# Optimization experiments

Measured on AMD Instinct MI355X. Metric: run time of the kernel, lower is better.

## Reference

```python
import jax, jax.numpy as jnp
import numpy as np

B, S, D = 2, 2048, 4096
NH, NKV = 32, 8
HD = D // NH          # 128
NREP = NH // NKV      # 4
THETA = 10000.0


def _rope_tables(seq_len, head_dim):
    inv = 1.0 / (THETA ** (jnp.arange(0, head_dim, 2, dtype=jnp.float32) / head_dim))  # [HD/2]
    t = jnp.arange(seq_len, dtype=jnp.float32)
    ang = jnp.outer(t, inv)                      # [S, HD/2]
    return jnp.cos(ang), jnp.sin(ang)


def _apply_rope(x, cos, sin):
    # x: [b, s, h, d]; interleaved pairs (even=real, odd=imag), matching view_as_complex
    xr = x.reshape(*x.shape[:-1], HD // 2, 2)
    x0, x1 = xr[..., 0], xr[..., 1]
    c = cos[None, :, None, :]
    s = sin[None, :, None, :]
    o0 = x0 * c - x1 * s
    o1 = x0 * s + x1 * c
    return jnp.stack([o0, o1], axis=-1).reshape(x.shape)


def setup_inputs() -> dict:
    key = jax.random.key(0)
    ks = jax.random.split(key, 5)
    sc = 0.02
    return {
        "x": jax.random.normal(ks[0], (B, S, D), jnp.float32),
        "wq": jax.random.normal(ks[1], (D, NH * HD), jnp.float32) * sc,
        "wk": jax.random.normal(ks[2], (D, NKV * HD), jnp.float32) * sc,
        "wv": jax.random.normal(ks[3], (D, NKV * HD), jnp.float32) * sc,
        "wo": jax.random.normal(ks[4], (NH * HD, D), jnp.float32) * sc,
        "start_pos": 0,
        "inference": 0,
    }


def reference(x, wq, wk, wv, wo, start_pos, inference):
    bsz, seq_len, _ = x.shape
    # QKV projections (training path: inference=False)
    xq = (x @ wq).reshape(bsz, seq_len, NH, HD)
    xk = (x @ wk).reshape(bsz, seq_len, NKV, HD)
    xv = (x @ wv).reshape(bsz, seq_len, NKV, HD)

    cos, sin = _rope_tables(seq_len, HD)
    xq = _apply_rope(xq, cos, sin)
    xk = _apply_rope(xk, cos, sin)

    # GQA without materializing repeated KV: group q heads per kv head
    q = xq.reshape(bsz, seq_len, NKV, NREP, HD)           # [b, s, g, r, d]
    scores = jnp.einsum('bqgrd,bkgd->bgrqk', q, xk) / np.sqrt(HD)
    causal = jnp.triu(jnp.full((seq_len, seq_len), -jnp.inf, jnp.float32), k=1)
    scores = scores + causal
    probs = jax.nn.softmax(scores.astype(jnp.float32), axis=-1).astype(x.dtype)
    out = jnp.einsum('bgrqk,bkgd->bqgrd', probs, xv)      # [b, s, g, r, d]
    out = out.reshape(bsz, seq_len, NH * HD)
    return out @ wo
```

## Files before the change

kernel.cpp:

```cpp
#include <hip/hip_runtime.h>
#include <hip/hip_bf16.h>

#define B_ 2
#define S_ 2048
#define D_ 4096
#define NH_ 32
#define NKV_ 8
#define HD_ 128
#define NREP_ 4

typedef unsigned short u16;
typedef __attribute__((ext_vector_type(8))) short short8;
typedef __attribute__((ext_vector_type(4))) float f32x4;

__device__ inline float bf2f(u16 u) {
    union { unsigned u; float f; } v; v.u = ((unsigned)u) << 16; return v.f;
}
__device__ inline u16 f2bf(float f) {
    union { float f; unsigned u; } v; v.f = f;
    unsigned r = v.u + 0x7fffu + ((v.u >> 16) & 1u);
    return (u16)(r >> 16);
}
__device__ inline unsigned cvt_pk(float lo, float hi) {
    unsigned r;
    asm("v_cvt_pk_bf16_f32 %0, %1, %2" : "=v"(r) : "v"(lo), "v"(hi));
    return r;
}
__device__ inline float exp2_fast(float x) {
    float r;
    asm("v_exp_f32 %0, %1" : "=v"(r) : "v"(x));
    return r;
}

__device__ inline void gl_lds16(const u16* g, u16* l) {
    __builtin_amdgcn_global_load_lds(
        (const __attribute__((address_space(1))) unsigned int*)g,
        (__attribute__((address_space(3))) unsigned int*)l, 16, 0, 0);
}

__global__ __launch_bounds__(256) void conv_k(const float* __restrict__ in,
                                              u16* __restrict__ out) {
    size_t i = ((size_t)blockIdx.x * 256 + threadIdx.x) * 4;
    float4 v = *(const float4*)&in[i];
    uint2 t;
    t.x = cvt_pk(v.x, v.y);
    t.y = cvt_pk(v.z, v.w);
    *(uint2*)&out[i] = t;
}

__global__ __launch_bounds__(256) void tconv_k(const float* __restrict__ in,
                                               u16* __restrict__ out,
                                               int R, int C) {
    __shared__ u16 tile[64][65];
    int bx = blockIdx.x * 64, by = blockIdx.y * 64;
    int tx = threadIdx.x, ty = threadIdx.y;
    for (int i = ty; i < 64; i += 4)
        tile[i][tx] = f2bf(in[(size_t)(by + i) * C + bx + tx]);
    __syncthreads();
    for (int i = ty; i < 64; i += 4)
        out[(size_t)(bx + i) * R + by + tx] = tile[tx][i];
}

__global__ __launch_bounds__(256) void tconv2_k(const float* __restrict__ in0,
                                                const float* __restrict__ in1,
                                                u16* __restrict__ out0,
                                                u16* __restrict__ out1,
                                                int R, int C) {
    __shared__ u16 tile[64][65];
    const float* in = blockIdx.z ? in1 : in0;
    u16* out = blockIdx.z ? out1 : out0;
    int bx = blockIdx.x * 64, by = blockIdx.y * 64;
    int tx = threadIdx.x, ty = threadIdx.y;
    for (int i = ty; i < 64; i += 4)
        tile[i][tx] = f2bf(in[(size_t)(by + i) * C + bx + tx]);
    __syncthreads();
    for (int i = ty; i < 64; i += 4)
        out[(size_t)(bx + i) * R + by + tx] = tile[tx][i];
}

__global__ __launch_bounds__(256) void transpose_k(const u16* __restrict__ in,
                                                   u16* __restrict__ out,
                                                   int R, int C) {
    __shared__ u16 tile[64][65];
    const u16* ib = in + (size_t)blockIdx.z * R * C;
    u16* ob = out + (size_t)blockIdx.z * R * C;
    int bx = blockIdx.x * 64, by = blockIdx.y * 64;
    int tx = threadIdx.x, ty = threadIdx.y;
    for (int i = ty; i < 64; i += 4)
        tile[i][tx] = ib[(size_t)(by + i) * C + bx + tx];
    __syncthreads();
    for (int i = ty; i < 64; i += 4)
        ob[(size_t)(bx + i) * R + by + tx] = tile[tx][i];
}

__global__ __launch_bounds__(256) void gemm_kv(const u16* __restrict__ A,
                                               const u16* __restrict__ Bt,
                                               u16* __restrict__ Kout,
                                               u16* __restrict__ Vout,
                                               int M, int K) {
    __shared__ __align__(16) u16 As[128 * 32];
    __shared__ __align__(16) u16 Bs[128 * 32];
    int tid = threadIdx.x;
    int w = tid >> 6, lane = tid & 63;
    int ln = lane & 15, qd = lane >> 4;
    int wr = w >> 1, wc = w & 1;
    int m0 = blockIdx.y * 128, n0 = blockIdx.x * 128;

    int srow = lane >> 2;
    int skk  = (lane & 3) * 8;
    const u16* Ag = A  + (size_t)(m0 + w * 32 + srow) * K + skk;
    const u16* Bg = Bt + (size_t)(n0 + w * 32 + srow) * K + skk;

    f32x4 acc[4][4];
#pragma unroll
    for (int i = 0; i < 4; ++i)
#pragma unroll
        for (int j = 0; j < 4; ++j)
            acc[i][j] = f32x4{0.f, 0.f, 0.f, 0.f};

    for (int k0 = 0; k0 < K; k0 += 32) {
#pragma unroll
        for (int t = 0; t < 2; ++t) {
            gl_lds16(Ag + (size_t)(t * 16) * K + k0, &As[(w * 32 + t * 16) * 32]);
            gl_lds16(Bg + (size_t)(t * 16) * K + k0, &Bs[(w * 32 + t * 16) * 32]);
        }
        __syncthreads();
        short8 af[4], bfr[4];
#pragma unroll
        for (int i = 0; i < 4; ++i)
            af[i] = *(const short8*)&As[(wr * 64 + i * 16 + ln) * 32 + qd * 8];
#pragma unroll
        for (int j = 0; j < 4; ++j)
            bfr[j] = *(const short8*)&Bs[(wc * 64 + j * 16 + ln) * 32 + qd * 8];
#pragma unroll
        for (int i = 0; i < 4; ++i)
#pragma unroll
            for (int j = 0; j < 4; ++j)
                acc[i][j] = __builtin_amdgcn_mfma_f32_16x16x32_bf16(af[i], bfr[j], acc[i][j], 0, 0, 0);
        __syncthreads();
    }
    u16* dst = (n0 < 1024) ? Kout : Vout;
    int nb = (n0 < 1024) ? n0 : (n0 - 1024);
#pragma unroll
    for (int i = 0; i < 4; ++i)
#pragma unroll
        for (int j = 0; j < 4; ++j)
#pragma unroll
            for (int r = 0; r < 4; ++r) {
                int row = m0 + wr * 64 + i * 16 + qd * 4 + r;
                int col = nb + wc * 64 + j * 16 + ln;
                dst[(size_t)row * 1024 + col] = f2bf(acc[i][j][r]);
            }
}

__device__ inline short8 lds_frag(const u16* base, int row, int colb) {
    int lin = ((row & 127) << 7) + colb;
    int off = ((row >> 7) << 14) + (lin ^ (((lin >> 9) & 1) << 5));
    return *(const short8*)((const char*)base + off);
}

__device__ inline void stage_half(const u16* g, int row0, int ldK, int k0,
                                  u16* ldsHalf, int w, int lane) {
#pragma unroll
    for (int j = 0; j < 2; ++j) {
        int Lb = (w << 11) + (j << 10) + (lane << 4);
        int src = Lb ^ (((Lb >> 9) & 1) << 5);
        const u16* gp = g + (size_t)(row0 + (src >> 7)) * ldK + k0 + ((src & 127) >> 1);
        gl_lds16(gp, ldsHalf + (((w << 11) + (j << 10)) >> 1));
    }
}

#define PH_MFMA(MB)                                                           \
    asm volatile("s_waitcnt lgkmcnt(0)" ::: "memory");                        \
    __builtin_amdgcn_sched_barrier(0);                                        \
    __builtin_amdgcn_s_setprio(1);                                            \
    _Pragma("unroll") for (int mi = 0; mi < 2; ++mi)                          \
      _Pragma("unroll") for (int ni = 0; ni < 4; ++ni)                        \
        _Pragma("unroll") for (int kk = 0; kk < 2; ++kk)                      \
          acc[(MB) + mi][ni] = __builtin_amdgcn_mfma_f32_16x16x32_bf16(       \
              af[mi][kk], bfr[ni][kk], acc[(MB) + mi][ni], 0, 0, 0);          \
    __builtin_amdgcn_s_setprio(0);                                            \
    __builtin_amdgcn_s_barrier();

#define TILE_BODY(T, CURA, CURB, OTHA)                                        \
  {                                                                           \
    const int t_ = (T);                                                       \
    const bool p1_ = (t_ + 1 < nt), p2_ = (t_ + 2 < nt);                      \
    short8 bfr[4][2], af[2][2];                                               \
    _Pragma("unroll") for (int ni = 0; ni < 4; ++ni)                          \
      _Pragma("unroll") for (int kk = 0; kk < 2; ++kk)                        \
        bfr[ni][kk] = lds_frag(CURB, wn * 64 + ni * 16 + ln, kk * 64 + qd * 16); \
    _Pragma("unroll") for (int mi = 0; mi < 2; ++mi)                          \
      _Pragma("unroll") for (int kk = 0; kk < 2; ++kk)                        \
        af[mi][kk] = lds_frag(CURA, wm * 128 + mi * 16 + ln, kk * 64 + qd * 16); \
    if (p1_) stage_half(Ag, 0, K, (t_ + 1) << 6, OTHA, w, lane);              \
    asm volatile("s_waitcnt lgkmcnt(8)" ::: "memory");                        \
    __builtin_amdgcn_s_barrier();                                             \
    PH_MFMA(0)                                                                \
    _Pragma("unroll") for (int mi = 0; mi < 2; ++mi)                          \
      _Pragma("unroll") for (int kk = 0; kk < 2; ++kk)                        \
        af[mi][kk] = lds_frag(CURA, wm * 128 + (mi + 2) * 16 + ln, kk * 64 + qd * 16); \
    if (p1_) stage_half(Ag, 128, K, (t_ + 1) << 6, OTHA + 8192, w, lane);     \
    __builtin_amdgcn_s_barrier();                                             \
    PH_MFMA(2)                                                                \
    _Pragma("unroll") for (int mi = 0; mi < 2; ++mi)                          \
      _Pragma("unroll") for (int kk = 0; kk < 2; ++kk)                        \
        af[mi][kk] = lds_frag(CURA, wm * 128 + (mi + 4) * 16 + ln, kk * 64 + qd * 16); \
    if (p2_) stage_half(Bg, 0, K, (t_ + 2) << 6, CURB, w, lane);              \
    __builtin_amdgcn_s_barrier();                                             \
    PH_MFMA(4)                                                                \
    _Pragma("unroll") for (int mi = 0; mi < 2; ++mi)                          \
      _Pragma("unroll") for (int kk = 0; kk < 2; ++kk)                        \
        af[mi][kk] = lds_frag(CURA, wm * 128 + (mi + 6) * 16 + ln, kk * 64 + qd * 16); \
    if (p2_) {                                                                \
        stage_half(Bg, 128, K, (t_ + 2) << 6, CURB + 8192, w, lane);          \
        asm volatile("s_waitcnt vmcnt(4)" ::: "memory");                      \
    } else if (p1_) {                                                         \
        asm volatile("s_waitcnt vmcnt(0)" ::: "memory");                      \
    }                                                                         \
    __builtin_amdgcn_s_barrier();                                             \
    PH_MFMA(6)                                                                \
  }

template <int OUT_F32>
__global__ __launch_bounds__(512, 1) void gemm256(const u16* __restrict__ A,
                                                  const u16* __restrict__ Bt,
                                                  void* __restrict__ Cv,
                                                  int M, int N, int K) {
    __shared__ __align__(16) u16 As[2][16384];
    __shared__ __align__(16) u16 Bs[2][16384];

    int tid = threadIdx.x;
    int w = tid >> 6, lane = tid & 63;
    int ln = lane & 15, qd = lane >> 4;
    int wm = w >> 2, wn = w & 3;

    int nbx = N >> 8;
    int cpx = gridDim.x >> 3;
    int bid = blockIdx.x;
    int swz = (bid & 7) * cpx + (bid >> 3);
    int m0 = (swz / nbx) << 8;
    int n0 = (swz % nbx) << 8;

    const u16* Ag = A + (size_t)m0 * K;
    const u16* Bg = Bt + (size_t)n0 * K;
    int nt = K >> 6;

    f32x4 acc[8][4];
#pragma unroll
    for (int i = 0; i < 8; ++i)
#pragma unroll
        for (int j = 0; j < 4; ++j) acc[i][j] = f32x4{0.f, 0.f, 0.f, 0.f};

    u16* A0 = &As[0][0]; u16* A1v = &As[1][0];
    u16* B0 = &Bs[0][0]; u16* B1v = &Bs[1][0];

    stage_half(Ag, 0,   K, 0,  A0,         w, lane);
    stage_half(Ag, 128, K, 0,  A0 + 8192,  w, lane);
    stage_half(Bg, 0,   K, 0,  B0,         w, lane);
    stage_half(Bg, 128, K, 0,  B0 + 8192,  w, lane);
    stage_half(Bg, 0,   K, 64, B1v,        w, lane);
    stage_half(Bg, 128, K, 64, B1v + 8192, w, lane);
    asm volatile("s_waitcnt vmcnt(4)" ::: "memory");
    __builtin_amdgcn_s_barrier();

    for (int tt = 0; tt < nt; tt += 2) {
        TILE_BODY(tt,     A0,  B0,  A1v)
        TILE_BODY(tt + 1, A1v, B1v, A0)
    }

#pragma unroll
    for (int mi = 0; mi < 8; ++mi)
#pragma unroll
        for (int ni = 0; ni < 4; ++ni)
#pragma unroll
            for (int r = 0; r < 4; ++r) {
                int row = m0 + wm * 128 + mi * 16 + qd * 4 + r;
                int col = n0 + wn * 64 + ni * 16 + ln;
                if (OUT_F32)
                    ((float*)Cv)[(size_t)row * N + col] = acc[mi][ni][r];
                else
                    ((u16*)Cv)[(size_t)row * N + col] = f2bf(acc[mi][ni][r]);
            }
}

__global__ __launch_bounds__(256) void rope_k(u16* __restrict__ Q,
                                              u16* __restrict__ Kb,
                                              float qscale) {
    const int ngq = B_ * S_ * NH_ * (HD_ / 8);
    const int ngk = B_ * S_ * NKV_ * (HD_ / 8);
    int i = blockIdx.x * 256 + threadIdx.x;
    u16* buf; int nheads; float scale;
    if (i < ngq) { buf = Q; nheads = NH_; scale = qscale; }
    else {
        i -= ngq;
        if (i >= ngk) return;
        buf = Kb; nheads = NKV_; scale = 1.f;
    }
    int gp = i & 15;
    int hh = (i >> 4) % nheads;
    int row = i / (16 * nheads);
    int s = row & (S_ - 1);
    size_t base = ((size_t)row * nheads + hh) * HD_ + gp * 8;
    uint4 v = *(const uint4*)&buf[base];
    unsigned ov[4];
    unsigned* vp = (unsigned*)&v;
#pragma unroll
    for (int j = 0; j < 4; ++j) {
        int p = gp * 4 + j;
        float freq = __expf(-(float)(2 * p) * (9.210340371976184f / 128.0f));
        float ang = (float)s * freq;
        float c, sn;
        sincosf(ang, &sn, &c);
        float x0 = bf2f((u16)vp[j]), x1 = bf2f((u16)(vp[j] >> 16));
        ov[j] = cvt_pk((x0 * c - x1 * sn) * scale, (x0 * sn + x1 * c) * scale);
    }
    *(uint4*)&buf[base] = *(uint4*)ov;
}

__global__ __launch_bounds__(512, 4) void attn_k(const u16* __restrict__ Q,
                                                 const u16* __restrict__ K,
                                                 const u16* __restrict__ Vt,
                                                 u16* __restrict__ AO) {
    __shared__ __align__(16) u16 Ks[2][64 * 128];
    __shared__ __align__(16) u16 Vts[2][128 * 64];

    int tid = threadIdx.x;
    int w = tid >> 6, lane = tid & 63;
    int ln = lane & 15, qd = lane >> 4;
    int sw = (ln & 7) << 4;

    int h  = blockIdx.y;
    int b  = blockIdx.z;
    int g  = h >> 2;

    const u16* Kbase = K + (size_t)(b * S_) * (NKV_ * HD_) + g * HD_;
    const u16* Vtb   = Vt + ((size_t)(b * NKV_ + g)) * HD_ * S_;

    int kr0 = tid >> 4;
    int kg0 = (tid & 15) * 8;
    int kcs = (kg0 * 2) ^ ((kr0 & 7) << 4);
    int vr0 = tid >> 3;
    int vg0 = (tid & 7) * 8;
    int vcs = (vg0 * 2) ^ ((vr0 & 7) << 4);

    for (int pass = 0; pass < 2; ++pass) {
        int qt = pass ? (S_ / 128 - 1 - (int)blockIdx.x) : (int)blockIdx.x;
        int q0 = qt * 128;
        int qb = q0 + w * 16;
        int qg = qb + ln;
        int ntw   = ((qb + 15) >> 6) + 1;
        int nfull = (qb + 1) >> 6;

        const u16* qptr = Q + ((size_t)(b * S_ + qg)) * (NH_ * HD_) + h * HD_;
        short8 bq[4];
#pragma unroll
        for (int kq = 0; kq < 4; ++kq)
            bq[kq] = *(const short8*)(qptr + kq * 32 + qd * 8);

        f32x4 ot[8];
#pragma unroll
        for (int db = 0; db < 8; ++db) ot[db] = f32x4{0.f, 0.f, 0.f, 0.f};
        float m_s = -1e30f, l_s = 0.f;

        int nk = 2 * qt + 2;

        {
            int4 a0 = *(const int4*)(Kbase + (size_t)kr0 * (NKV_ * HD_) + kg0);
            int4 a1 = *(const int4*)(Kbase + (size_t)(kr0 + 32) * (NKV_ * HD_) + kg0);
            int4 v0 = *(const int4*)(Vtb + (size_t)vr0 * S_ + vg0);
            int4 v1 = *(const int4*)(Vtb + (size_t)(vr0 + 64) * S_ + vg0);
            *(int4*)((char*)&Ks[0][0] + kr0 * 256 + kcs) = a0;
            *(int4*)((char*)&Ks[0][0] + (kr0 + 32) * 256 + kcs) = a1;
            *(int4*)((char*)&Vts[0][0] + vr0 * 128 + vcs) = v0;
            *(int4*)((char*)&Vts[0][0] + (vr0 + 64) * 128 + vcs) = v1;
        }
        __syncthreads();

        for (int kt = 0; kt < nk; ++kt) {
            int bb = kt & 1;
            int k0 = kt * 64;
            bool pf = (kt + 1 < nk);
            int4 pa0, pa1, pv0, pv1;
            if (pf) {
                int k0n = k0 + 64;
                pa0 = *(const int4*)(Kbase + (size_t)(k0n + kr0) * (NKV_ * HD_) + kg0);
                pa1 = *(const int4*)(Kbase + (size_t)(k0n + kr0 + 32) * (NKV_ * HD_) + kg0);
                pv0 = *(const int4*)(Vtb + (size_t)vr0 * S_ + k0n + vg0);
                pv1 = *(const int4*)(Vtb + (size_t)(vr0 + 64) * S_ + k0n + vg0);
            }

            if (kt < ntw) {
                f32x4 st[4];
#pragma unroll
                for (int kb = 0; kb < 4; ++kb) st[kb] = f32x4{0.f, 0.f, 0.f, 0.f};
                __builtin_amdgcn_s_setprio(1);
#pragma unroll
                for (int kb = 0; kb < 4; ++kb)
#pragma unroll
                    for (int kq = 0; kq < 4; ++kq) {
                        short8 ak = *(const short8*)((const char*)&Ks[bb][0] +
                                    (kb * 16 + ln) * 256 + ((kq * 64 + qd * 16) ^ sw));
                        st[kb] = __builtin_amdgcn_mfma_f32_16x16x32_bf16(ak, bq[kq], st[kb], 0, 0, 0);
                    }
                __builtin_amdgcn_s_setprio(0);

                float mx;
                if (kt >= nfull) {
                    int lim = qg - k0 - qd * 4;
                    mx = -1e30f;
#pragma unroll
                    for (int kb = 0; kb < 4; ++kb)
#pragma unroll
                        for (int r = 0; r < 4; ++r) {
                            if (16 * kb + r > lim) st[kb][r] = -1e30f;
                            mx = fmaxf(mx, st[kb][r]);
                        }
                } else {
                    mx = st[0][0];
#pragma unroll
                    for (int kb = 0; kb < 4; ++kb)
#pragma unroll
                        for (int r = 0; r < 4; ++r)
                            if (kb + r) mx = fmaxf(mx, st[kb][r]);
                }
                mx = fmaxf(mx, __shfl_xor(mx, 16, 64));
                mx = fmaxf(mx, __shfl_xor(mx, 32, 64));

                if (__any(mx > m_s + 8.f)) {
                    float mn = fmaxf(m_s, mx);
                    float alpha = exp2_fast(m_s - mn);
                    m_s = mn;
                    l_s *= alpha;
#pragma unroll
                    for (int db = 0; db < 8; ++db)
#pragma unroll
                        for (int r = 0; r < 4; ++r) ot[db][r] *= alpha;
                }
                float rs = 0.f;
#pragma unroll
                for (int kb = 0; kb < 4; ++kb)
#pragma unroll
                    for (int r = 0; r < 4; ++r) {
                        float pv = exp2_fast(st[kb][r] - m_s);
                        st[kb][r] = pv;
                        rs += pv;
                    }
                rs += __shfl_xor(rs, 16, 64);
                rs += __shfl_xor(rs, 32, 64);
                l_s += rs;

                unsigned pk[4][2];
#pragma unroll
                for (int kb = 0; kb < 4; ++kb) {
                    pk[kb][0] = cvt_pk(st[kb][0], st[kb][1]);
                    pk[kb][1] = cvt_pk(st[kb][2], st[kb][3]);
                }
                int sA = ((qd & 1) << 5) + ln;
                int sB = sA + 16;
                bool hi = (qd & 2) != 0;
#pragma unroll
                for (int ks = 0; ks < 2; ++ks) {
                    unsigned t0a = (unsigned)__shfl((int)pk[2 * ks][0], sA, 64);
                    unsigned t0b = (unsigned)__shfl((int)pk[2 * ks][1], sA, 64);
                    unsigned t1a = (unsigned)__shfl((int)pk[2 * ks + 1][0], sA, 64);
                    unsigned t1b = (unsigned)__shfl((int)pk[2 * ks + 1][1], sA, 64);
                    unsigned t2a = (unsigned)__shfl((int)pk[2 * ks][0], sB, 64);
                    unsigned t2b = (unsigned)__shfl((int)pk[2 * ks][1], sB, 64);
                    unsigned t3a = (unsigned)__shfl((int)pk[2 * ks + 1][0], sB, 64);
                    unsigned t3b = (unsigned)__shfl((int)pk[2 * ks + 1][1], sB, 64);
                    union { unsigned u[4]; short8 s8; } bp;
                    bp.u[0] = hi ? t1a : t0a;
                    bp.u[1] = hi ? t1b : t0b;
                    bp.u[2] = hi ? t3a : t2a;
                    bp.u[3] = hi ? t3b : t2b;
                    __builtin_amdgcn_s_setprio(1);
#pragma unroll
                    for (int db = 0; db < 8; ++db) {
                        short8 av = *(const short8*)((const char*)&Vts[bb][0] +
                                    (db * 16 + ln) * 128 + ((ks * 64 + qd * 16) ^ sw));
                        ot[db] = __builtin_amdgcn_mfma_f32_16x16x32_bf16(av, bp.s8, ot[db], 0, 0, 0);
                    }
                    __builtin_amdgcn_s_setprio(0);
                }
            }

            if (pf) {
                int nb2 = bb ^ 1;
                *(int4*)((char*)&Ks[nb2][0] + kr0 * 256 + kcs) = pa0;
                *(int4*)((char*)&Ks[nb2][0] + (kr0 + 32) * 256 + kcs) = pa1;
                *(int4*)((char*)&Vts[nb2][0] + vr0 * 128 + vcs) = pv0;
                *(int4*)((char*)&Vts[nb2][0] + (vr0 + 64) * 128 + vcs) = pv1;
            }
            __syncthreads();
        }

        float invl = 1.0f / l_s;
        size_t orow = (size_t)(b * S_ + qg) * (NH_ * HD_) + h * HD_;
#pragma unroll
        for (int db = 0; db < 8; ++db) {
            uint2 t2;
            t2.x = cvt_pk(ot[db][0] * invl, ot[db][1] * invl);
            t2.y = cvt_pk(ot[db][2] * invl, ot[db][3] * invl);
            *(uint2*)&AO[orow + db * 16 + qd * 4] = t2;
        }
    }
}

extern "C" void kernel_launch(void* const* d_in, const int* in_sizes, int n_in,
                              void* d_out, int out_size, void* d_ws, size_t ws_size,
                              hipStream_t stream) {
    const float* x  = (const float*)d_in[0];
    const float* wq = (const float*)d_in[1];
    const float* wk = (const float*)d_in[2];
    const float* wv = (const float*)d_in[3];
    const float* wo = (const float*)d_in[4];
    float* out = (float*)d_out;

    char* p = (char*)d_ws;
    auto alloc = [&](size_t nelem) { u16* r = (u16*)p; p += nelem * 2; return r; };
    u16* xb  = alloc(4096ull * 4096);
    u16* wqT = alloc(4096ull * 4096);
    u16* wkT = alloc(1024ull * 4096);
    u16* wvT = alloc(1024ull * 4096);
    u16* Q   = alloc(4096ull * 4096);
    u16* Kb  = alloc(4096ull * 1024);
    u16* Vb  = alloc(4096ull * 1024);
    u16* AO  = alloc(4096ull * 4096);

    dim3 tblk(64, 4);
    conv_k<<<16384, 256, 0, stream>>>(x, xb);
    tconv_k<<<dim3(64, 64), tblk, 0, stream>>>(wq, wqT, 4096, 4096);
    tconv2_k<<<dim3(16, 64, 2), tblk, 0, stream>>>(wk, wv, wkT, wvT, 4096, 1024);

    gemm256<0><<<256, 512, 0, stream>>>(xb, wqT, Q, 4096, 4096, 4096);
    gemm_kv<<<dim3(16, 32), 256, 0, stream>>>(xb, wkT, Kb, Vb, 4096, 4096);

    u16* woT = xb;
    u16* Vt  = wqT;
    tconv_k<<<dim3(64, 64), tblk, 0, stream>>>(wo, woT, 4096, 4096);

    int ng = B_ * S_ * NH_ * (HD_ / 8) + B_ * S_ * NKV_ * (HD_ / 8);
    rope_k<<<(ng + 255) / 256, 256, 0, stream>>>(Q, Kb, 0.12751743f);

    transpose_k<<<dim3(16, 32, 2), tblk, 0, stream>>>(Vb, Vt, S_, NKV_ * HD_);

    attn_k<<<dim3(S_ / 256, NH_, B_), 512, 0, stream>>>(Q, Kb, Vt, AO);

    gemm256<1><<<256, 512, 0, stream>>>(AO, woT, out, 4096, 4096, 4096);
}
```

Measured before the change: 727.9 us.

## Route K/V projection through pipelined 256-tile GEMM and change LDS swizzle

Removes the simple 128x128 single-buffered gemm_kv kernel and computes the fused K/V projection with the pipelined gemm256 kernel using a new output mode that splits columns into the K and V buffers. It relies on wkT and wvT being contiguous, which makes them one 2048-column weight. It also replaces the LDS XOR swizzle with a row-based (row&7)<<4 pattern to cut bank conflicts in fragment loads for all gemm256 uses. The risks are that a 128-block grid underfills the GPU and that the new swizzle must match between staging and reading.

```diff
diff --git a/kernel.cpp b/kernel.cpp
--- a/kernel.cpp
+++ b/kernel.cpp
@@ -93,69 +93,9 @@
         ob[(size_t)(bx + i) * R + by + tx] = tile[tx][i];
 }
 
-__global__ __launch_bounds__(256) void gemm_kv(const u16* __restrict__ A,
-                                               const u16* __restrict__ Bt,
-                                               u16* __restrict__ Kout,
-                                               u16* __restrict__ Vout,
-                                               int M, int K) {
-    __shared__ __align__(16) u16 As[128 * 32];
-    __shared__ __align__(16) u16 Bs[128 * 32];
-    int tid = threadIdx.x;
-    int w = tid >> 6, lane = tid & 63;
-    int ln = lane & 15, qd = lane >> 4;
-    int wr = w >> 1, wc = w & 1;
-    int m0 = blockIdx.y * 128, n0 = blockIdx.x * 128;
-
-    int srow = lane >> 2;
-    int skk  = (lane & 3) * 8;
-    const u16* Ag = A  + (size_t)(m0 + w * 32 + srow) * K + skk;
-    const u16* Bg = Bt + (size_t)(n0 + w * 32 + srow) * K + skk;
-
-    f32x4 acc[4][4];
-#pragma unroll
-    for (int i = 0; i < 4; ++i)
-#pragma unroll
-        for (int j = 0; j < 4; ++j)
-            acc[i][j] = f32x4{0.f, 0.f, 0.f, 0.f};
-
-    for (int k0 = 0; k0 < K; k0 += 32) {
-#pragma unroll
-        for (int t = 0; t < 2; ++t) {
-            gl_lds16(Ag + (size_t)(t * 16) * K + k0, &As[(w * 32 + t * 16) * 32]);
-            gl_lds16(Bg + (size_t)(t * 16) * K + k0, &Bs[(w * 32 + t * 16) * 32]);
-        }
-        __syncthreads();
-        short8 af[4], bfr[4];
-#pragma unroll
-        for (int i = 0; i < 4; ++i)
-            af[i] = *(const short8*)&As[(wr * 64 + i * 16 + ln) * 32 + qd * 8];
-#pragma unroll
-        for (int j = 0; j < 4; ++j)
-            bfr[j] = *(const short8*)&Bs[(wc * 64 + j * 16 + ln) * 32 + qd * 8];
-#pragma unroll
-        for (int i = 0; i < 4; ++i)
-#pragma unroll
-            for (int j = 0; j < 4; ++j)
-                acc[i][j] = __builtin_amdgcn_mfma_f32_16x16x32_bf16(af[i], bfr[j], acc[i][j], 0, 0, 0);
-        __syncthreads();
-    }
-    u16* dst = (n0 < 1024) ? Kout : Vout;
-    int nb = (n0 < 1024) ? n0 : (n0 - 1024);
-#pragma unroll
-    for (int i = 0; i < 4; ++i)
-#pragma unroll
-        for (int j = 0; j < 4; ++j)
-#pragma unroll
-            for (int r = 0; r < 4; ++r) {
-                int row = m0 + wr * 64 + i * 16 + qd * 4 + r;
-                int col = nb + wc * 64 + j * 16 + ln;
-                dst[(size_t)row * 1024 + col] = f2bf(acc[i][j][r]);
-            }
-}
 
 __device__ inline short8 lds_frag(const u16* base, int row, int colb) {
-    int lin = ((row & 127) << 7) + colb;
-    int off = ((row >> 7) << 14) + (lin ^ (((lin >> 9) & 1) << 5));
+    int off = ((row >> 7) << 14) + ((row & 127) << 7) + (colb ^ ((row & 7) << 4));
     return *(const short8*)((const char*)base + off);
 }
 
@@ -164,8 +104,9 @@
 #pragma unroll
     for (int j = 0; j < 2; ++j) {
         int Lb = (w << 11) + (j << 10) + (lane << 4);
-        int src = Lb ^ (((Lb >> 9) & 1) << 5);
-        const u16* gp = g + (size_t)(row0 + (src >> 7)) * ldK + k0 + ((src & 127) >> 1);
+        int r  = Lb >> 7;
+        int c  = (Lb & 127) ^ ((r & 7) << 4);
+        const u16* gp = g + (size_t)(row0 + r) * ldK + k0 + (c >> 1);
         gl_lds16(gp, ldsHalf + (((w << 11) + (j << 10)) >> 1));
     }
 }
@@ -222,7 +163,7 @@
     PH_MFMA(6)                                                                \
   }
 
-template <int OUT_F32>
+template <int OUT_MODE>
 __global__ __launch_bounds__(512, 1) void gemm256(const u16* __restrict__ A,
                                                   const u16* __restrict__ Bt,
                                                   void* __restrict__ Cv,
@@ -277,10 +218,14 @@
             for (int r = 0; r < 4; ++r) {
                 int row = m0 + wm * 128 + mi * 16 + qd * 4 + r;
                 int col = n0 + wn * 64 + ni * 16 + ln;
-                if (OUT_F32)
+                if (OUT_MODE == 1)
                     ((float*)Cv)[(size_t)row * N + col] = acc[mi][ni][r];
-                else
+                else if (OUT_MODE == 0)
                     ((u16*)Cv)[(size_t)row * N + col] = f2bf(acc[mi][ni][r]);
+                else {
+                    u16* dst = (u16*)Cv + ((col < 1024) ? 0 : (4096ull * 1024 - 1024));
+                    dst[(size_t)row * 1024 + col] = f2bf(acc[mi][ni][r]);
+                }
             }
 }
 
@@ -534,7 +479,7 @@
     tconv2_k<<<dim3(16, 64, 2), tblk, 0, stream>>>(wk, wv, wkT, wvT, 4096, 1024);
 
     gemm256<0><<<256, 512, 0, stream>>>(xb, wqT, Q, 4096, 4096, 4096);
-    gemm_kv<<<dim3(16, 32), 256, 0, stream>>>(xb, wkT, Kb, Vb, 4096, 4096);
+    gemm256<2><<<128, 512, 0, stream>>>(xb, wkT, Kb, 4096, 2048, 4096);
 
     u16* woT = xb;
     u16* Vt  = wqT;
```

New measurement: 724.7 us. About the same (-0.4%).
